# Kernel optimization log

Hardware: AMD Instinct MI355X
Metric: run time of the kernel (lower is better)

The kernel has to match this reference:

```python
import jax, jax.numpy as jnp
import numpy as np

N_NODES = 100000
N_EDGES = 1600000
IN_FEAT = 256
HIDDEN = 64
N_CLASSES = 16


def gcn_conv(x, edge_index, W, b):
    """PyG GCNConv: add self-loops, symmetric normalization, linear+aggregate."""
    n = x.shape[0]
    src, dst = edge_index[0], edge_index[1]
    loops = jnp.arange(n, dtype=src.dtype)
    src = jnp.concatenate([src, loops])
    dst = jnp.concatenate([dst, loops])
    # in-degree on graph with self-loops
    deg = jax.ops.segment_sum(jnp.ones(src.shape[0], dtype=x.dtype), dst, num_segments=n)
    dinv = jnp.where(deg > 0, jax.lax.rsqrt(deg), 0.0)
    h = x @ W                                  # [N, out]
    norm = dinv[src] * dinv[dst]               # [E+N]
    msg = h[src] * norm[:, None]                # gather + scale (memory-bound)
    out = jax.ops.segment_sum(msg, dst, num_segments=n)  # scatter-add
    return out + b


def setup_inputs() -> dict:
    key = jax.random.key(0)
    ks = jax.random.split(key, 5)
    x = jax.random.normal(ks[0], (N_NODES, IN_FEAT), dtype=jnp.float32)
    edge_index = jax.random.randint(ks[1], (2, N_EDGES), 0, N_NODES, dtype=jnp.int64)
    W1 = jax.random.normal(ks[2], (IN_FEAT, HIDDEN), dtype=jnp.float32) * (1.0 / np.sqrt(IN_FEAT))
    b1 = jnp.zeros((HIDDEN,), dtype=jnp.float32)
    W2 = jax.random.normal(ks[3], (HIDDEN, N_CLASSES), dtype=jnp.float32) * (1.0 / np.sqrt(HIDDEN))
    b2 = jnp.zeros((N_CLASSES,), dtype=jnp.float32)
    return {"x": x, "edge_index": edge_index, "W1": W1, "b1": b1, "W2": W2, "b2": b2}


def reference(x, edge_index, W1, b1, W2, b2):
    h = gcn_conv(x, edge_index, W1, b1)
    h = jax.nn.relu(h)
    # dropout p=0.5 is identity in eval mode (training=False)
    out = gcn_conv(h, edge_index, W2, b2)
    return out
```

## Files before the change

### kernel.cpp

```cpp
#include <hip/hip_runtime.h>

#define NN 100000
#define NE 1600000
#define FIN 256
#define FH 64
#define FC 16

#define SCAN_CHUNK 1024
#define NB_SCAN ((NN + SCAN_CHUNK - 1) / SCAN_CHUNK)
#define NSWEEP 4
#define SWEEP_W ((NN + NSWEEP - 1) / NSWEEP)

typedef int v4i __attribute__((ext_vector_type(4)));

__global__ void detect_k(const int* __restrict__ ei, int* __restrict__ flag) {
    if (threadIdx.x == 0 && blockIdx.x == 0) {
        int z = (ei[1] == 0) & (ei[3] == 0) & (ei[5] == 0) & (ei[7] == 0);
        *flag = z;
    }
}

__device__ __forceinline__ int eidx(const int* __restrict__ ei, int f, int pos) {
    return f ? ei[2 * pos] : ei[pos];
}

__global__ __launch_bounds__(256) void count_k(const int* __restrict__ ei,
                                               const int* __restrict__ flag,
                                               int* __restrict__ deg,
                                               v4i* __restrict__ packed) {
    int e = blockIdx.x * 256 + threadIdx.x;
    if (e >= NE) return;
    int f = *flag;
    int s = eidx(ei, f, e);
    int d = eidx(ei, f, NE + e);
    int r = atomicAdd(&deg[d], 1);
    v4i p; p.x = s; p.y = d; p.z = r; p.w = 0;
    packed[e] = p;
}

__global__ void dinv_k(const int* __restrict__ deg, float* __restrict__ dinv) {
    int i = blockIdx.x * 256 + threadIdx.x;
    if (i < NN) dinv[i] = rsqrtf((float)(deg[i] + 1));
}

__global__ __launch_bounds__(256) void scan_sum_k(const int* __restrict__ deg,
                                                  int* __restrict__ partial) {
    __shared__ int red[256];
    int b = blockIdx.x, t = threadIdx.x;
    int base = b * SCAN_CHUNK + t * 4;
    int s = 0;
    #pragma unroll
    for (int i = 0; i < 4; i++) { int idx = base + i; if (idx < NN) s += deg[idx]; }
    red[t] = s;
    __syncthreads();
    for (int off = 128; off > 0; off >>= 1) {
        if (t < off) red[t] += red[t + off];
        __syncthreads();
    }
    if (t == 0) partial[b] = red[0];
}

__global__ __launch_bounds__(128) void scan_part_k(int* __restrict__ partial) {
    __shared__ int s[128];
    int t = threadIdx.x;
    int v = (t < NB_SCAN) ? partial[t] : 0;
    s[t] = v; __syncthreads();
    for (int off = 1; off < 128; off <<= 1) {
        int u = (t >= off) ? s[t - off] : 0;
        __syncthreads();
        s[t] += u;
        __syncthreads();
    }
    if (t < NB_SCAN) partial[t] = s[t] - v;
}

__global__ __launch_bounds__(256) void scan_out_k(const int* __restrict__ deg,
                                                  const int* __restrict__ partial,
                                                  int* __restrict__ row_start) {
    __shared__ int s[256];
    int b = blockIdx.x, t = threadIdx.x;
    int base = b * SCAN_CHUNK + t * 4;
    int v[4]; int sum = 0;
    #pragma unroll
    for (int i = 0; i < 4; i++) {
        int idx = base + i;
        v[i] = (idx < NN) ? deg[idx] : 0;
        sum += v[i];
    }
    s[t] = sum; __syncthreads();
    for (int off = 1; off < 256; off <<= 1) {
        int u = (t >= off) ? s[t - off] : 0;
        __syncthreads();
        s[t] += u;
        __syncthreads();
    }
    int run = partial[b] + s[t] - sum;
    #pragma unroll
    for (int i = 0; i < 4; i++) {
        int idx = base + i;
        if (idx < NN) {
            row_start[idx] = run;
            run += v[i];
            if (idx == NN - 1) row_start[NN] = run;
        }
    }
}

__global__ __launch_bounds__(256) void fill_k(const v4i* __restrict__ packed,
                                              const int* __restrict__ row_start,
                                              int* __restrict__ csr,
                                              int lo, int hi) {
    int e = blockIdx.x * 256 + threadIdx.x;
    if (e >= NE) return;
    v4i p = __builtin_nontemporal_load(&packed[e]);
    if (p.y < lo || p.y >= hi) return;
    csr[row_start[p.y] + p.z] = p.x;
}

__global__ __launch_bounds__(256) void gemm1_k(const float* __restrict__ x,
                                               const float* __restrict__ W,
                                               float* __restrict__ h) {
    __shared__ float As[64][68];
    __shared__ float Bs[64][64];
    const int t = threadIdx.x;
    const int r0 = blockIdx.x * 64;
    const int tx4 = (t & 15) * 4;
    const int ty4 = (t >> 4) * 4;
    const int lrow = t >> 4;
    const int lkf = (t & 15) * 4;

    float acc[4][4] = {};

    for (int k0 = 0; k0 < FIN; k0 += 64) {
        #pragma unroll
        for (int i = 0; i < 4; i++) {
            int row = lrow + 16 * i;
            int gr = r0 + row;
            float4 v = make_float4(0.f, 0.f, 0.f, 0.f);
            if (gr < NN) v = *(const float4*)&x[gr * FIN + k0 + lkf];
            As[lkf + 0][row] = v.x;
            As[lkf + 1][row] = v.y;
            As[lkf + 2][row] = v.z;
            As[lkf + 3][row] = v.w;
            float4 w = *(const float4*)&W[(k0 + row) * FH + lkf];
            *(float4*)&Bs[row][lkf] = w;
        }
        __syncthreads();
        #pragma unroll 8
        for (int kk = 0; kk < 64; kk++) {
            float4 a = *(const float4*)&As[kk][ty4];
            float4 b = *(const float4*)&Bs[kk][tx4];
            float av[4] = {a.x, a.y, a.z, a.w};
            float bv[4] = {b.x, b.y, b.z, b.w};
            #pragma unroll
            for (int i2 = 0; i2 < 4; i2++)
                #pragma unroll
                for (int j2 = 0; j2 < 4; j2++)
                    acc[i2][j2] = fmaf(av[i2], bv[j2], acc[i2][j2]);
        }
        __syncthreads();
    }
    #pragma unroll
    for (int i2 = 0; i2 < 4; i2++) {
        int r = r0 + ty4 + i2;
        if (r < NN)
            *(float4*)&h[r * FH + tx4] =
                make_float4(acc[i2][0], acc[i2][1], acc[i2][2], acc[i2][3]);
    }
}

__global__ __launch_bounds__(256) void agg1_k(const int* __restrict__ csr,
                                              const int* __restrict__ row_start,
                                              const float* __restrict__ h1,
                                              const float* __restrict__ dinv,
                                              const float* __restrict__ b1,
                                              float* __restrict__ agg) {
    int n = blockIdx.x * 4 + (threadIdx.x >> 6);
    int lane = threadIdx.x & 63;
    if (n >= NN) return;
    int s0 = row_start[n], s1 = row_start[n + 1];
    float acc = 0.f, a0 = 0.f, a1 = 0.f, a2 = 0.f, a3 = 0.f;
    for (int j0 = s0; j0 < s1; j0 += 64) {
        int idx = j0 + lane;
        int sl = 0; float wl = 0.f;
        if (idx < s1) { sl = csr[idx]; wl = dinv[sl]; }
        int cnt = s1 - j0; if (cnt > 64) cnt = 64;
        int j = 0;
        for (; j + 4 <= cnt; j += 4) {
            int   sA = __shfl(sl, j + 0, 64), sB = __shfl(sl, j + 1, 64);
            int   sC = __shfl(sl, j + 2, 64), sD = __shfl(sl, j + 3, 64);
            float wA = __shfl(wl, j + 0, 64), wB = __shfl(wl, j + 1, 64);
            float wC = __shfl(wl, j + 2, 64), wD = __shfl(wl, j + 3, 64);
            float hA = h1[sA * FH + lane];
            float hB = h1[sB * FH + lane];
            float hC = h1[sC * FH + lane];
            float hD = h1[sD * FH + lane];
            a0 = fmaf(hA, wA, a0); a1 = fmaf(hB, wB, a1);
            a2 = fmaf(hC, wC, a2); a3 = fmaf(hD, wD, a3);
        }
        for (; j < cnt; j++) {
            int   s = __shfl(sl, j, 64);
            float w = __shfl(wl, j, 64);
            acc = fmaf(h1[s * FH + lane], w, acc);
        }
    }
    acc += (a0 + a1) + (a2 + a3);
    float dn = dinv[n];
    acc = fmaf(h1[n * FH + lane], dn, acc);
    agg[n * FH + lane] = fmaf(acc, dn, b1[lane]);
}

__global__ __launch_bounds__(192) void gemm2_k(const float* __restrict__ agg,
                                               const float* __restrict__ W2,
                                               float* __restrict__ h2) {
    __shared__ float a_lds[192 * 65];
    const int t = threadIdx.x;
    const int r0 = blockIdx.x * 192;
    #pragma unroll
    for (int i = 0; i < 16; i++) {
        int fidx = t + 192 * i;
        int row = fidx >> 4, kf = (fidx & 15) * 4;
        int gr = r0 + row;
        float4 v = make_float4(0.f, 0.f, 0.f, 0.f);
        if (gr < NN) v = *(const float4*)&agg[gr * FH + kf];
        v.x = fmaxf(v.x, 0.f); v.y = fmaxf(v.y, 0.f);
        v.z = fmaxf(v.z, 0.f); v.w = fmaxf(v.w, 0.f);
        a_lds[row * 65 + kf + 0] = v.x;
        a_lds[row * 65 + kf + 1] = v.y;
        a_lds[row * 65 + kf + 2] = v.z;
        a_lds[row * 65 + kf + 3] = v.w;
    }
    __syncthreads();
    float acc[FC] = {};
    #pragma unroll 4
    for (int k = 0; k < FH; k++) {
        float a = a_lds[t * 65 + k];
        #pragma unroll
        for (int c = 0; c < FC; c++)
            acc[c] = fmaf(a, W2[k * FC + c], acc[c]);
    }
    int r = r0 + t;
    if (r < NN) {
        #pragma unroll
        for (int q = 0; q < 4; q++)
            *(float4*)&h2[r * FC + 4 * q] =
                make_float4(acc[4*q], acc[4*q+1], acc[4*q+2], acc[4*q+3]);
    }
}

__global__ __launch_bounds__(256) void agg2_k(const int* __restrict__ csr,
                                              const int* __restrict__ row_start,
                                              const float* __restrict__ h2,
                                              const float* __restrict__ dinv,
                                              const float* __restrict__ b2,
                                              float* __restrict__ out) {
    int n = blockIdx.x * 16 + (threadIdx.x >> 4);
    int l16 = threadIdx.x & 15;
    int base = threadIdx.x & 48;
    if (n >= NN) return;
    int s0 = row_start[n], s1 = row_start[n + 1];
    float acc = 0.f, a0 = 0.f, a1 = 0.f, a2 = 0.f, a3 = 0.f;
    for (int j0 = s0; j0 < s1; j0 += 16) {
        int idx = j0 + l16;
        int sl = 0; float wl = 0.f;
        if (idx < s1) { sl = csr[idx]; wl = dinv[sl]; }
        int cnt = s1 - j0; if (cnt > 16) cnt = 16;
        int j = 0;
        for (; j + 4 <= cnt; j += 4) {
            int   sA = __shfl(sl, base + j + 0, 64), sB = __shfl(sl, base + j + 1, 64);
            int   sC = __shfl(sl, base + j + 2, 64), sD = __shfl(sl, base + j + 3, 64);
            float wA = __shfl(wl, base + j + 0, 64), wB = __shfl(wl, base + j + 1, 64);
            float wC = __shfl(wl, base + j + 2, 64), wD = __shfl(wl, base + j + 3, 64);
            float hA = h2[sA * FC + l16];
            float hB = h2[sB * FC + l16];
            float hC = h2[sC * FC + l16];
            float hD = h2[sD * FC + l16];
            a0 = fmaf(hA, wA, a0); a1 = fmaf(hB, wB, a1);
            a2 = fmaf(hC, wC, a2); a3 = fmaf(hD, wD, a3);
        }
        for (; j < cnt; j++) {
            int   s = __shfl(sl, base + j, 64);
            float w = __shfl(wl, base + j, 64);
            acc = fmaf(h2[s * FC + l16], w, acc);
        }
    }
    acc += (a0 + a1) + (a2 + a3);
    float dn = dinv[n];
    acc = fmaf(h2[n * FC + l16], dn, acc);
    out[n * FC + l16] = fmaf(acc, dn, b2[l16]);
}

extern "C" void kernel_launch(void* const* d_in, const int* in_sizes, int n_in,
                              void* d_out, int out_size, void* d_ws, size_t ws_size,
                              hipStream_t stream) {
    const float* x  = (const float*)d_in[0];
    const int*   ei = (const int*)d_in[1];
    const float* W1 = (const float*)d_in[2];
    const float* b1 = (const float*)d_in[3];
    const float* W2 = (const float*)d_in[4];
    const float* b2 = (const float*)d_in[5];
    float* out = (float*)d_out;

    char* ws = (char*)d_ws;
    int*   deg       = (int*)(ws + 0);
    int*   row_start = (int*)(ws + 512 * 1024);
    float* dinv      = (float*)(ws + 1024 * 1024);
    int*   flag      = (int*)(ws + 1536 * 1024);
    int*   partial   = (int*)(ws + 1540 * 1024);
    int*   csr       = (int*)(ws + 2ull * 1024 * 1024);
    v4i*   packed    = (v4i*)(ws + 9ull * 1024 * 1024);
    float* h1        = (float*)(ws + 9ull * 1024 * 1024);
    float* agg1      = (float*)(ws + 35ull * 1024 * 1024);
    float* h2        = h1;

    detect_k<<<1, 64, 0, stream>>>(ei, flag);
    (void)hipMemsetAsync(deg, 0, NN * sizeof(int), stream);
    count_k<<<(NE + 255) / 256, 256, 0, stream>>>(ei, flag, deg, packed);
    dinv_k<<<(NN + 255) / 256, 256, 0, stream>>>(deg, dinv);
    scan_sum_k<<<NB_SCAN, 256, 0, stream>>>(deg, partial);
    scan_part_k<<<1, 128, 0, stream>>>(partial);
    scan_out_k<<<NB_SCAN, 256, 0, stream>>>(deg, partial, row_start);
    for (int sw = 0; sw < NSWEEP; sw++)
        fill_k<<<(NE + 255) / 256, 256, 0, stream>>>(packed, row_start, csr,
                                                     sw * SWEEP_W, (sw + 1) * SWEEP_W);

    gemm1_k<<<(NN + 63) / 64, 256, 0, stream>>>(x, W1, h1);
    agg1_k<<<(NN + 3) / 4, 256, 0, stream>>>(csr, row_start, h1, dinv, b1, agg1);

    gemm2_k<<<(NN + 191) / 192, 192, 0, stream>>>(agg1, W2, h2);
    agg2_k<<<(NN + 15) / 16, 256, 0, stream>>>(csr, row_start, h2, dinv, b2, out);
}
```

Before: 423.9 us.

## Fuse edge counting with first GEMM and pack edge records into 8 bytes

Merges the degree-counting kernel and the first dense GEMM into one launch, with block ranges selecting the role, so the memory-bound atomic counting overlaps the compute-bound GEMM. The per-edge record shrinks from 16 to 8 bytes by packing the destination (17 bits) and its rank within that destination into one int. The fill pass drops from four sweeps to two. The packed buffer moves to the agg1 region so it no longer overlaps h1, and the rank field assumes in-degree stays below 2^15.

```diff
diff --git a/kernel.cpp b/kernel.cpp
--- a/kernel.cpp
+++ b/kernel.cpp
@@ -8,10 +8,12 @@
 
 #define SCAN_CHUNK 1024
 #define NB_SCAN ((NN + SCAN_CHUNK - 1) / SCAN_CHUNK)
-#define NSWEEP 4
+#define NSWEEP 2
 #define SWEEP_W ((NN + NSWEEP - 1) / NSWEEP)
-
-typedef int v4i __attribute__((ext_vector_type(4)));
+#define NB_COUNT ((NE + 255) / 256)
+#define NB_GEMM1 ((NN + 63) / 64)
+
+typedef int v2i __attribute__((ext_vector_type(2)));
 
 __global__ void detect_k(const int* __restrict__ ei, int* __restrict__ flag) {
     if (threadIdx.x == 0 && blockIdx.x == 0) {
@@ -24,106 +26,28 @@
     return f ? ei[2 * pos] : ei[pos];
 }
 
-__global__ __launch_bounds__(256) void count_k(const int* __restrict__ ei,
+__global__ __launch_bounds__(256) void fused_k(const int* __restrict__ ei,
                                                const int* __restrict__ flag,
                                                int* __restrict__ deg,
-                                               v4i* __restrict__ packed) {
-    int e = blockIdx.x * 256 + threadIdx.x;
-    if (e >= NE) return;
-    int f = *flag;
-    int s = eidx(ei, f, e);
-    int d = eidx(ei, f, NE + e);
-    int r = atomicAdd(&deg[d], 1);
-    v4i p; p.x = s; p.y = d; p.z = r; p.w = 0;
-    packed[e] = p;
-}
-
-__global__ void dinv_k(const int* __restrict__ deg, float* __restrict__ dinv) {
-    int i = blockIdx.x * 256 + threadIdx.x;
-    if (i < NN) dinv[i] = rsqrtf((float)(deg[i] + 1));
-}
-
-__global__ __launch_bounds__(256) void scan_sum_k(const int* __restrict__ deg,
-                                                  int* __restrict__ partial) {
-    __shared__ int red[256];
-    int b = blockIdx.x, t = threadIdx.x;
-    int base = b * SCAN_CHUNK + t * 4;
-    int s = 0;
-    #pragma unroll
-    for (int i = 0; i < 4; i++) { int idx = base + i; if (idx < NN) s += deg[idx]; }
-    red[t] = s;
-    __syncthreads();
-    for (int off = 128; off > 0; off >>= 1) {
-        if (t < off) red[t] += red[t + off];
-        __syncthreads();
-    }
-    if (t == 0) partial[b] = red[0];
-}
-
-__global__ __launch_bounds__(128) void scan_part_k(int* __restrict__ partial) {
-    __shared__ int s[128];
-    int t = threadIdx.x;
-    int v = (t < NB_SCAN) ? partial[t] : 0;
-    s[t] = v; __syncthreads();
-    for (int off = 1; off < 128; off <<= 1) {
-        int u = (t >= off) ? s[t - off] : 0;
-        __syncthreads();
-        s[t] += u;
-        __syncthreads();
-    }
-    if (t < NB_SCAN) partial[t] = s[t] - v;
-}
-
-__global__ __launch_bounds__(256) void scan_out_k(const int* __restrict__ deg,
-                                                  const int* __restrict__ partial,
-                                                  int* __restrict__ row_start) {
-    __shared__ int s[256];
-    int b = blockIdx.x, t = threadIdx.x;
-    int base = b * SCAN_CHUNK + t * 4;
-    int v[4]; int sum = 0;
-    #pragma unroll
-    for (int i = 0; i < 4; i++) {
-        int idx = base + i;
-        v[i] = (idx < NN) ? deg[idx] : 0;
-        sum += v[i];
-    }
-    s[t] = sum; __syncthreads();
-    for (int off = 1; off < 256; off <<= 1) {
-        int u = (t >= off) ? s[t - off] : 0;
-        __syncthreads();
-        s[t] += u;
-        __syncthreads();
-    }
-    int run = partial[b] + s[t] - sum;
-    #pragma unroll
-    for (int i = 0; i < 4; i++) {
-        int idx = base + i;
-        if (idx < NN) {
-            row_start[idx] = run;
-            run += v[i];
-            if (idx == NN - 1) row_start[NN] = run;
-        }
-    }
-}
-
-__global__ __launch_bounds__(256) void fill_k(const v4i* __restrict__ packed,
-                                              const int* __restrict__ row_start,
-                                              int* __restrict__ csr,
-                                              int lo, int hi) {
-    int e = blockIdx.x * 256 + threadIdx.x;
-    if (e >= NE) return;
-    v4i p = __builtin_nontemporal_load(&packed[e]);
-    if (p.y < lo || p.y >= hi) return;
-    csr[row_start[p.y] + p.z] = p.x;
-}
-
-__global__ __launch_bounds__(256) void gemm1_k(const float* __restrict__ x,
+                                               v2i* __restrict__ packed,
+                                               const float* __restrict__ x,
                                                const float* __restrict__ W,
                                                float* __restrict__ h) {
+    if (blockIdx.x < NB_COUNT) {
+        int e = blockIdx.x * 256 + threadIdx.x;
+        if (e >= NE) return;
+        int f = *flag;
+        int s = eidx(ei, f, e);
+        int d = eidx(ei, f, NE + e);
+        int r = atomicAdd(&deg[d], 1);
+        v2i p; p.x = s; p.y = d | (r << 17);
+        packed[e] = p;
+        return;
+    }
     __shared__ float As[64][68];
     __shared__ float Bs[64][64];
     const int t = threadIdx.x;
-    const int r0 = blockIdx.x * 64;
+    const int r0 = (blockIdx.x - NB_COUNT) * 64;
     const int tx4 = (t & 15) * 4;
     const int ty4 = (t >> 4) * 4;
     const int lrow = t >> 4;
@@ -167,6 +91,87 @@
             *(float4*)&h[r * FH + tx4] =
                 make_float4(acc[i2][0], acc[i2][1], acc[i2][2], acc[i2][3]);
     }
+}
+
+__global__ void dinv_k(const int* __restrict__ deg, float* __restrict__ dinv) {
+    int i = blockIdx.x * 256 + threadIdx.x;
+    if (i < NN) dinv[i] = rsqrtf((float)(deg[i] + 1));
+}
+
+__global__ __launch_bounds__(256) void scan_sum_k(const int* __restrict__ deg,
+                                                  int* __restrict__ partial) {
+    __shared__ int red[256];
+    int b = blockIdx.x, t = threadIdx.x;
+    int base = b * SCAN_CHUNK + t * 4;
+    int s = 0;
+    #pragma unroll
+    for (int i = 0; i < 4; i++) { int idx = base + i; if (idx < NN) s += deg[idx]; }
+    red[t] = s;
+    __syncthreads();
+    for (int off = 128; off > 0; off >>= 1) {
+        if (t < off) red[t] += red[t + off];
+        __syncthreads();
+    }
+    if (t == 0) partial[b] = red[0];
+}
+
+__global__ __launch_bounds__(128) void scan_part_k(int* __restrict__ partial) {
+    __shared__ int s[128];
+    int t = threadIdx.x;
+    int v = (t < NB_SCAN) ? partial[t] : 0;
+    s[t] = v; __syncthreads();
+    for (int off = 1; off < 128; off <<= 1) {
+        int u = (t >= off) ? s[t - off] : 0;
+        __syncthreads();
+        s[t] += u;
+        __syncthreads();
+    }
+    if (t < NB_SCAN) partial[t] = s[t] - v;
+}
+
+__global__ __launch_bounds__(256) void scan_out_k(const int* __restrict__ deg,
+                                                  const int* __restrict__ partial,
+                                                  int* __restrict__ row_start) {
+    __shared__ int s[256];
+    int b = blockIdx.x, t = threadIdx.x;
+    int base = b * SCAN_CHUNK + t * 4;
+    int v[4]; int sum = 0;
+    #pragma unroll
+    for (int i = 0; i < 4; i++) {
+        int idx = base + i;
+        v[i] = (idx < NN) ? deg[idx] : 0;
+        sum += v[i];
+    }
+    s[t] = sum; __syncthreads();
+    for (int off = 1; off < 256; off <<= 1) {
+        int u = (t >= off) ? s[t - off] : 0;
+        __syncthreads();
+        s[t] += u;
+        __syncthreads();
+    }
+    int run = partial[b] + s[t] - sum;
+    #pragma unroll
+    for (int i = 0; i < 4; i++) {
+        int idx = base + i;
+        if (idx < NN) {
+            row_start[idx] = run;
+            run += v[i];
+            if (idx == NN - 1) row_start[NN] = run;
+        }
+    }
+}
+
+__global__ __launch_bounds__(256) void fill_k(const v2i* __restrict__ packed,
+                                              const int* __restrict__ row_start,
+                                              int* __restrict__ csr,
+                                              int lo, int hi) {
+    int e = blockIdx.x * 256 + threadIdx.x;
+    if (e >= NE) return;
+    v2i p = __builtin_nontemporal_load(&packed[e]);
+    int d = p.y & 0x1FFFF;
+    if (d < lo || d >= hi) return;
+    int r = ((unsigned)p.y) >> 17;
+    csr[row_start[d] + r] = p.x;
 }
 
 __global__ __launch_bounds__(256) void agg1_k(const int* __restrict__ csr,
@@ -308,14 +313,14 @@
     int*   flag      = (int*)(ws + 1536 * 1024);
     int*   partial   = (int*)(ws + 1540 * 1024);
     int*   csr       = (int*)(ws + 2ull * 1024 * 1024);
-    v4i*   packed    = (v4i*)(ws + 9ull * 1024 * 1024);
     float* h1        = (float*)(ws + 9ull * 1024 * 1024);
+    v2i*   packed    = (v2i*)(ws + 35ull * 1024 * 1024);
     float* agg1      = (float*)(ws + 35ull * 1024 * 1024);
     float* h2        = h1;
 
     detect_k<<<1, 64, 0, stream>>>(ei, flag);
     (void)hipMemsetAsync(deg, 0, NN * sizeof(int), stream);
-    count_k<<<(NE + 255) / 256, 256, 0, stream>>>(ei, flag, deg, packed);
+    fused_k<<<NB_COUNT + NB_GEMM1, 256, 0, stream>>>(ei, flag, deg, packed, x, W1, h1);
     dinv_k<<<(NN + 255) / 256, 256, 0, stream>>>(deg, dinv);
     scan_sum_k<<<NB_SCAN, 256, 0, stream>>>(deg, partial);
     scan_part_k<<<1, 128, 0, stream>>>(partial);
@@ -324,9 +329,7 @@
         fill_k<<<(NE + 255) / 256, 256, 0, stream>>>(packed, row_start, csr,
                                                      sw * SWEEP_W, (sw + 1) * SWEEP_W);
 
-    gemm1_k<<<(NN + 63) / 64, 256, 0, stream>>>(x, W1, h1);
     agg1_k<<<(NN + 3) / 4, 256, 0, stream>>>(csr, row_start, h1, dinv, b1, agg1);
-
     gemm2_k<<<(NN + 191) / 192, 192, 0, stream>>>(agg1, W2, h2);
     agg2_k<<<(NN + 15) / 16, 256, 0, stream>>>(csr, row_start, h2, dinv, b2, out);
 }
```

Result: faster. 398.0 us (-6.1%).
